# Kernel optimization log

Hardware: AMD Instinct MI355X
Metric: run time of the kernel (lower is better)

Reference implementation:

```python
import jax, jax.numpy as jnp
import numpy as np

EMB = 1024
N_HEAD = 16
HEAD = 64
D_FF = 4 * EMB
LN_EPS = 1e-5


def layernorm(x, g, b):
    mu = jnp.mean(x, axis=-1, keepdims=True)
    var = jnp.mean(jnp.square(x - mu), axis=-1, keepdims=True)
    return (x - mu) * jax.lax.rsqrt(var + LN_EPS) * g + b


def setup_inputs() -> dict:
    key = jax.random.key(0)
    ks = jax.random.split(key, 12)
    s = 0.02
    x = jax.random.normal(ks[0], (4, 2048, EMB), dtype=jnp.float32)
    # per-head Q/K/V projections (no bias), stacked along head axis
    Wq = jax.random.normal(ks[1], (N_HEAD, EMB, HEAD), dtype=jnp.float32) * s
    Wk = jax.random.normal(ks[2], (N_HEAD, EMB, HEAD), dtype=jnp.float32) * s
    Wv = jax.random.normal(ks[3], (N_HEAD, EMB, HEAD), dtype=jnp.float32) * s
    Wo = jax.random.normal(ks[4], (EMB, EMB), dtype=jnp.float32) * s
    bo = jnp.zeros((EMB,), dtype=jnp.float32)
    ln1_g = jnp.ones((EMB,), dtype=jnp.float32)
    ln1_b = jnp.zeros((EMB,), dtype=jnp.float32)
    W1 = jax.random.normal(ks[5], (EMB, D_FF), dtype=jnp.float32) * s
    b1 = jnp.zeros((D_FF,), dtype=jnp.float32)
    W2 = jax.random.normal(ks[6], (D_FF, EMB), dtype=jnp.float32) * s
    b2 = jnp.zeros((EMB,), dtype=jnp.float32)
    ln2_g = jnp.ones((EMB,), dtype=jnp.float32)
    ln2_b = jnp.zeros((EMB,), dtype=jnp.float32)
    return dict(x=x, Wq=Wq, Wk=Wk, Wv=Wv, Wo=Wo, bo=bo, ln1_g=ln1_g,
                ln1_b=ln1_b, W1=W1, b1=b1, W2=W2, b2=b2, ln2_g=ln2_g,
                ln2_b=ln2_b)


def reference(x, Wq, Wk, Wv, Wo, bo, ln1_g, ln1_b, W1, b1, W2, b2, ln2_g, ln2_b):
    B, T, _ = x.shape
    # fused multi-head QKV (equivalent to the per-head Python loop + concat)
    q = jnp.einsum('btd,hdk->bhtk', x, Wq)
    k = jnp.einsum('btd,hdk->bhtk', x, Wk)
    v = jnp.einsum('btd,hdk->bhtk', x, Wv)
    scores = jnp.einsum('bhtk,bhsk->bhts', q, k) / jnp.sqrt(jnp.float32(HEAD))
    att = jax.nn.softmax(scores, axis=-1)
    heads = jnp.einsum('bhts,bhsk->bhtk', att, v)           # [B,H,T,head]
    cat = heads.transpose(0, 2, 1, 3).reshape(B, T, EMB)     # concat over heads
    mha = cat @ Wo + bo
    x = x + layernorm(mha, ln1_g, ln1_b)                     # residual of LN(sublayer)
    ff = jax.nn.gelu(x @ W1 + b1, approximate=False) @ W2 + b2
    x = x + layernorm(ff, ln2_g, ln2_b)
    return x
```

## Files before the change

kernel.cpp:

```cpp
#include <hip/hip_runtime.h>
#include <math.h>


using u16 = unsigned short;
typedef __bf16 bf16x8 __attribute__((ext_vector_type(8)));
typedef __bf16 bf16x4 __attribute__((ext_vector_type(4)));
typedef unsigned short u16x8 __attribute__((ext_vector_type(8)));
typedef unsigned short u16x4 __attribute__((ext_vector_type(4)));
typedef float f32x4 __attribute__((ext_vector_type(4)));

#if defined(__has_builtin)
#if __has_builtin(__builtin_amdgcn_exp2f)
#define EXP2F(x) __builtin_amdgcn_exp2f(x)
#endif
#endif
#ifndef EXP2F
#define EXP2F(x) __expf((x) * 0.69314718055994531f)
#endif

__device__ __forceinline__ float bf2f(u16 h) {
  return __uint_as_float(((unsigned int)h) << 16);
}
__device__ __forceinline__ u16 f2bf(float f) {
  unsigned int u = __float_as_uint(f);
  u += 0x7fffu + ((u >> 16) & 1u);
  return (u16)(u >> 16);
}

__device__ __forceinline__ void gload_lds16(const void* g, void* l) {
  __builtin_amdgcn_global_load_lds(
      (__attribute__((address_space(1))) void*)(g),
      (__attribute__((address_space(3))) void*)(l), 16, 0, 0);
}

__global__ __launch_bounds__(256) void detect_dtype(const u16* __restrict__ x,
                                                    int* __restrict__ flag) {
  __shared__ int cnt[256];
  int c = 0;
#pragma unroll
  for (int j = 0; j < 8; ++j) {
    float v = bf2f(x[threadIdx.x * 8 + j]);
    float a = fabsf(v);
    if (a >= 1e-4f && a <= 64.0f) ++c;
  }
  cnt[threadIdx.x] = c;
  __syncthreads();
  if (threadIdx.x == 0) {
    int t = 0;
    for (int i = 0; i < 256; ++i) t += cnt[i];
    flag[0] = (t < 1638) ? 1 : 0;
  }
}

__global__ __launch_bounds__(256) void cvt_copy(const void* __restrict__ in,
                                                u16* __restrict__ out,
                                                const int* __restrict__ flagp,
                                                long n) {
  long idx = ((long)blockIdx.x * 256 + threadIdx.x) * 4;
  if (idx >= n) return;
  if (*flagp) {
    float4 v = *(const float4*)((const float*)in + idx);
    out[idx] = f2bf(v.x); out[idx + 1] = f2bf(v.y);
    out[idx + 2] = f2bf(v.z); out[idx + 3] = f2bf(v.w);
  } else {
    *(u16x4*)(out + idx) = *(const u16x4*)((const u16*)in + idx);
  }
}

__global__ __launch_bounds__(256) void cvt_vecs(
    const void* s0, const void* s1, const void* s2, const void* s3,
    const void* s4, const void* s5, const void* s6, u16* __restrict__ dst,
    const int* __restrict__ flagp) {
  const int lens[7] = {1024, 1024, 1024, 4096, 1024, 1024, 1024};
  const int offs[7] = {0, 1024, 2048, 3072, 7168, 8192, 9216};
  const void* srcs[7] = {s0, s1, s2, s3, s4, s5, s6};
  int w = blockIdx.x;
  int f = *flagp;
  for (int i = threadIdx.x; i < lens[w]; i += 256)
    dst[offs[w] + i] = f ? f2bf(((const float*)srcs[w])[i])
                         : ((const u16*)srcs[w])[i];
}

__global__ __launch_bounds__(256) void transpose_cvt(
    const void* __restrict__ in, u16* __restrict__ out, int R, int C,
    long inBS, long outBS, const int* __restrict__ flagp) {
  __shared__ u16 tile[32][33];
  int f = *flagp;
  u16* ob = out + (long)blockIdx.z * outBS;
  int c = blockIdx.x * 32 + threadIdx.x;
  int r0 = blockIdx.y * 32;
  if (f) {
    const float* ib = (const float*)in + (long)blockIdx.z * inBS;
#pragma unroll
    for (int i = threadIdx.y; i < 32; i += 8)
      tile[i][threadIdx.x] = f2bf(ib[(long)(r0 + i) * C + c]);
  } else {
    const u16* ib = (const u16*)in + (long)blockIdx.z * inBS;
#pragma unroll
    for (int i = threadIdx.y; i < 32; i += 8)
      tile[i][threadIdx.x] = ib[(long)(r0 + i) * C + c];
  }
  __syncthreads();
  int r = r0 + threadIdx.x;
  int c0 = blockIdx.x * 32;
#pragma unroll
  for (int i = threadIdx.y; i < 32; i += 8)
    ob[(long)(c0 + i) * R + r] = tile[threadIdx.x][i];
}

__global__ __launch_bounds__(256) void kv_frag(const u16* __restrict__ qkv,
                                               u16* __restrict__ KF,
                                               u16* __restrict__ VF) {
  __shared__ u16 Kt[64][72];
  __shared__ u16 Vt[64][72];
  const int jblk = blockIdx.x, bh = blockIdx.y;
  const int b = bh >> 4, h = bh & 15;
  const int tid = threadIdx.x;
  const long j0 = jblk * 64;

  {
    int tt = tid >> 2, c0 = (tid & 3) * 16;
    const u16* src = qkv + (long)(b * 2048 + j0 + tt) * 3072 + h * 64 + c0;
    *(u16x8*)(&Kt[tt][c0]) = *(const u16x8*)(src + 1024);
    *(u16x8*)(&Kt[tt][c0 + 8]) = *(const u16x8*)(src + 1024 + 8);
    *(u16x8*)(&Vt[tt][c0]) = *(const u16x8*)(src + 2048);
    *(u16x8*)(&Vt[tt][c0 + 8]) = *(const u16x8*)(src + 2048 + 8);
  }
  __syncthreads();

  long obase = ((long)bh * 32 + jblk) * 8 * 512;
#pragma unroll
  for (int si = 0; si < 2; ++si) {
    int s = tid * 2 + si;
    int f = s >> 6, ln = s & 63;
    int kt = f >> 2, nt = f & 3;
    int lr = ln & 15, lq = ln >> 4;
    u16x8 ko, vo;
#pragma unroll
    for (int j = 0; j < 8; ++j) {
      ko[j] = Kt[nt * 16 + lr][kt * 32 + lq * 8 + j];
      vo[j] = Vt[kt * 32 + lq * 8 + j][nt * 16 + lr];
    }
    *(u16x8*)(KF + obase + (long)s * 8) = ko;
    *(u16x8*)(VF + obase + (long)s * 8) = vo;
  }
}

template <int EPI>
__global__ __launch_bounds__(256) void gemm_bt(
    const u16* __restrict__ A, const u16* __restrict__ Bt,
    const u16* __restrict__ bias, void* __restrict__ Cout,
    int M, int N, int K) {
  __shared__ u16 As[128 * 32];
  __shared__ u16 Bs[128 * 32];
  const int tid = threadIdx.x;
  const int wave = tid >> 6, lane = tid & 63;
  const int m0 = blockIdx.x * 128, n0 = blockIdx.y * 128;
  const int wm = (wave >> 1) * 64, wn = (wave & 1) * 64;
  const int srow = lane >> 2, skoff = (lane & 3) * 8;

  const u16* ag[2];
  const u16* bg[2];
  u16* al[2];
  u16* bl[2];
#pragma unroll
  for (int p = 0; p < 2; ++p) {
    int r = p * 64 + wave * 16;
    ag[p] = A + (long)(m0 + r + srow) * K + skoff;
    bg[p] = Bt + (long)(n0 + r + srow) * K + skoff;
    al[p] = As + r * 32;
    bl[p] = Bs + r * 32;
  }

  f32x4 acc[4][4] = {};
  const int lr = lane & 15, lk = (lane >> 4) * 8;

  for (int k0 = 0; k0 < K; k0 += 32) {
#pragma unroll
    for (int p = 0; p < 2; ++p) {
      gload_lds16(ag[p] + k0, al[p]);
      gload_lds16(bg[p] + k0, bl[p]);
    }
    __syncthreads();
    bf16x8 af[4], bfr[4];
#pragma unroll
    for (int t = 0; t < 4; ++t) {
      af[t] = *(const bf16x8*)(As + (wm + t * 16 + lr) * 32 + lk);
      bfr[t] = *(const bf16x8*)(Bs + (wn + t * 16 + lr) * 32 + lk);
    }
#pragma unroll
    for (int mt = 0; mt < 4; ++mt)
#pragma unroll
      for (int nt = 0; nt < 4; ++nt)
        acc[mt][nt] = __builtin_amdgcn_mfma_f32_16x16x32_bf16(
            af[mt], bfr[nt], acc[mt][nt], 0, 0, 0);
    __syncthreads();
  }

  const int rq = (lane >> 4) * 4, cl = lane & 15;
#pragma unroll
  for (int mt = 0; mt < 4; ++mt)
#pragma unroll
    for (int nt = 0; nt < 4; ++nt) {
      int col = n0 + wn + nt * 16 + cl;
#pragma unroll
      for (int r = 0; r < 4; ++r) {
        long row = (long)(m0 + wm + mt * 16 + rq + r);
        float v = acc[mt][nt][r];
        if (EPI == 0) {
          ((u16*)Cout)[row * N + col] = f2bf(v);
        } else if (EPI == 2) {
          v += bf2f(bias[col]);
          v = 0.5f * v * (1.0f + erff(v * 0.70710678118654752f));
          ((u16*)Cout)[row * N + col] = f2bf(v);
        } else {
          v += bf2f(bias[col]);
          ((u16*)Cout)[row * N + col] = f2bf(v);
        }
      }
    }
}

__global__ __launch_bounds__(256) void flash_attn(
    const u16* __restrict__ qkv, const u16* __restrict__ KF,
    const u16* __restrict__ VF, u16* __restrict__ cat) {
  const int T = 2048, LD = 3072;
  const float QSCALE = 0.18033688011112042f;
  const float EXPC = 4.3280851226677321f;
  const int bh = blockIdx.y;
  const int b = bh >> 4, h = bh & 15;
  const int tid = threadIdx.x, wave = tid >> 6, lane = tid & 63;
  const int lr = lane & 15, lq = lane >> 4;

  __shared__ u16 Ps[4 * 32 * 72];
  u16* Pw = Ps + wave * 32 * 72;

  const u16* Qb = qkv + (long)(b * 2048) * LD + h * 64;
  const long fbase = (long)bh * 32 * 8 * 512;

  bf16x8 aq[2][2];
#pragma unroll
  for (int st = 0; st < 2; ++st) {
    int qrow = blockIdx.x * 128 + wave * 32 + st * 16 + lr;
#pragma unroll
    for (int kt = 0; kt < 2; ++kt) {
      u16x8 q = *(const u16x8*)(Qb + (long)qrow * LD + kt * 32 + lq * 8);
      bf16x8 t;
#pragma unroll
      for (int j = 0; j < 8; ++j) t[j] = (__bf16)(bf2f(q[j]) * QSCALE);
      aq[st][kt] = t;
    }
  }

  f32x4 o[2][4] = {};
  float lsum[2] = {0.0f, 0.0f};

  for (int jblk = 0; jblk < T / 64; ++jblk) {
    const u16* kf = KF + fbase + (long)jblk * 8 * 512;
    const u16* vf = VF + fbase + (long)jblk * 8 * 512;

    bf16x8 bk[2][4];
#pragma unroll
    for (int kt = 0; kt < 2; ++kt)
#pragma unroll
      for (int nt = 0; nt < 4; ++nt)
        bk[kt][nt] = *(const bf16x8*)(kf + (kt * 4 + nt) * 512 + lane * 8);

    f32x4 s[2][4] = {};
#pragma unroll
    for (int st = 0; st < 2; ++st)
#pragma unroll
      for (int nt = 0; nt < 4; ++nt)
#pragma unroll
        for (int kt = 0; kt < 2; ++kt)
          s[st][nt] = __builtin_amdgcn_mfma_f32_16x16x32_bf16(
              bk[kt][nt], aq[st][kt], s[st][nt], 0, 0, 0);

    bf16x8 bv[2][4];
#pragma unroll
    for (int kt = 0; kt < 2; ++kt)
#pragma unroll
      for (int nt = 0; nt < 4; ++nt)
        bv[kt][nt] = *(const bf16x8*)(vf + (kt * 4 + nt) * 512 + lane * 8);

#pragma unroll
    for (int st = 0; st < 2; ++st)
#pragma unroll
      for (int nt = 0; nt < 4; ++nt) {
        f32x4 p;
#pragma unroll
        for (int r = 0; r < 4; ++r) p[r] = EXP2F(s[st][nt][r] - EXPC);
        lsum[st] += (p[0] + p[1]) + (p[2] + p[3]);
        bf16x4 pk;
#pragma unroll
        for (int r = 0; r < 4; ++r) pk[r] = (__bf16)p[r];
        *(bf16x4*)(Pw + (st * 16 + lr) * 72 + nt * 16 + lq * 4) = pk;
      }

#pragma unroll
    for (int st = 0; st < 2; ++st)
#pragma unroll
      for (int kt = 0; kt < 2; ++kt) {
        bf16x8 ap =
            *(const bf16x8*)(Pw + (st * 16 + lr) * 72 + kt * 32 + lq * 8);
#pragma unroll
        for (int nt = 0; nt < 4; ++nt)
          o[st][nt] = __builtin_amdgcn_mfma_f32_16x16x32_bf16(
              ap, bv[kt][nt], o[st][nt], 0, 0, 0);
      }
  }

#pragma unroll
  for (int st = 0; st < 2; ++st) {
    lsum[st] += __shfl_xor(lsum[st], 16, 64);
    lsum[st] += __shfl_xor(lsum[st], 32, 64);
  }

  u16* ob = cat + (long)(b * 2048) * 1024 + h * 64;
#pragma unroll
  for (int st = 0; st < 2; ++st) {
    int trow = blockIdx.x * 128 + wave * 32 + st * 16 + lq * 4;
#pragma unroll
    for (int r = 0; r < 4; ++r) {
      float linv = 1.0f / __shfl(lsum[st], lq * 4 + r, 64);
#pragma unroll
      for (int nt = 0; nt < 4; ++nt)
        ob[(long)(trow + r) * 1024 + nt * 16 + lr] = f2bf(o[st][nt][r] * linv);
    }
  }
}

__global__ __launch_bounds__(256) void ln_residual(
    const u16* __restrict__ y, const void* __restrict__ res, int res_raw,
    const u16* __restrict__ g, const u16* __restrict__ bb,
    void* __restrict__ out, const int* __restrict__ flagp, int final_out) {
  const long row = blockIdx.x;
  const int tid = threadIdx.x, wave = tid >> 6, lane = tid & 63;
  u16x4 yv = *(const u16x4*)(y + row * 1024 + tid * 4);
  float yy[4];
#pragma unroll
  for (int j = 0; j < 4; ++j) yy[j] = bf2f(yv[j]);
  float s1 = yy[0] + yy[1] + yy[2] + yy[3];
  float s2 = yy[0] * yy[0] + yy[1] * yy[1] + yy[2] * yy[2] + yy[3] * yy[3];
#pragma unroll
  for (int off = 1; off < 64; off <<= 1) {
    s1 += __shfl_xor(s1, off, 64);
    s2 += __shfl_xor(s2, off, 64);
  }
  __shared__ float ws1[4], ws2[4];
  if (lane == 0) { ws1[wave] = s1; ws2[wave] = s2; }
  __syncthreads();
  float t1 = ws1[0] + ws1[1] + ws1[2] + ws1[3];
  float t2 = ws2[0] + ws2[1] + ws2[2] + ws2[3];
  float mu = t1 * (1.0f / 1024.0f);
  float var = t2 * (1.0f / 1024.0f) - mu * mu;
  float rstd = rsqrtf(var + 1e-5f);
  int i = tid * 4;
  bool f32in = res_raw && (*flagp);
  bool f32out = final_out && (*flagp);
#pragma unroll
  for (int j = 0; j < 4; ++j) {
    float rv = f32in ? ((const float*)res)[row * 1024 + i + j]
                     : bf2f(((const u16*)res)[row * 1024 + i + j]);
    float o = rv + (yy[j] - mu) * rstd * bf2f(g[i + j]) + bf2f(bb[i + j]);
    if (f32out)
      ((float*)out)[row * 1024 + i + j] = o;
    else
      ((u16*)out)[row * 1024 + i + j] = f2bf(o);
  }
}

extern "C" void kernel_launch(void* const* d_in, const int* in_sizes, int n_in,
                              void* d_out, int out_size, void* d_ws,
                              size_t ws_size, hipStream_t stream) {
  const void* x_raw = d_in[0];
  const void* Wq = d_in[1];
  const void* Wk = d_in[2];
  const void* Wv = d_in[3];
  const void* Wo = d_in[4];
  const void* bo = d_in[5];
  const void* ln1g = d_in[6];
  const void* ln1b = d_in[7];
  const void* W1 = d_in[8];
  const void* b1 = d_in[9];
  const void* W2 = d_in[10];
  const void* b2 = d_in[11];
  const void* ln2g = d_in[12];
  const void* ln2b = d_in[13];

  char* ws = (char*)d_ws;
  u16* qkv = (u16*)(ws + 0);
  u16* mha = (u16*)(ws + 0);
  u16* h1 = (u16*)(ws + 0);
  u16* cat = (u16*)(ws + 50331648);
  u16* KF = (u16*)(ws + 67108864);
  u16* ff = (u16*)(ws + 67108864);
  u16* xb = (u16*)(ws + 83886080);
  u16* VF = (u16*)(ws + 83886080);
  u16* x1 = (u16*)(ws + 83886080);
  u16* wqkvt = (u16*)(ws + 100663296);
  u16* wot = (u16*)(ws + 106954752);
  u16* w1t = (u16*)(ws + 109051904);
  u16* w2t = (u16*)(ws + 117440512);
  u16* vecs = (u16*)(ws + 125829120);
  int* flag = (int*)(ws + 125853696);

  const u16* v_bo = vecs + 0;
  const u16* v_l1g = vecs + 1024;
  const u16* v_l1b = vecs + 2048;
  const u16* v_b1 = vecs + 3072;
  const u16* v_b2 = vecs + 7168;
  const u16* v_l2g = vecs + 8192;
  const u16* v_l2b = vecs + 9216;

  detect_dtype<<<1, 256, 0, stream>>>((const u16*)x_raw, flag);
  cvt_copy<<<8192, 256, 0, stream>>>(x_raw, xb, flag, 8388608L);
  cvt_vecs<<<7, 256, 0, stream>>>(bo, ln1g, ln1b, b1, b2, ln2g, ln2b, vecs, flag);

  dim3 tb(32, 8);
  transpose_cvt<<<dim3(2, 32, 16), tb, 0, stream>>>(Wq, wqkvt, 1024, 64, 65536, 65536, flag);
  transpose_cvt<<<dim3(2, 32, 16), tb, 0, stream>>>(Wk, wqkvt + 1048576, 1024, 64, 65536, 65536, flag);
  transpose_cvt<<<dim3(2, 32, 16), tb, 0, stream>>>(Wv, wqkvt + 2097152, 1024, 64, 65536, 65536, flag);
  transpose_cvt<<<dim3(32, 32, 1), tb, 0, stream>>>(Wo, wot, 1024, 1024, 0, 0, flag);
  transpose_cvt<<<dim3(128, 32, 1), tb, 0, stream>>>(W1, w1t, 1024, 4096, 0, 0, flag);
  transpose_cvt<<<dim3(32, 128, 1), tb, 0, stream>>>(W2, w2t, 4096, 1024, 0, 0, flag);

  gemm_bt<0><<<dim3(64, 24), 256, 0, stream>>>(xb, wqkvt, nullptr, qkv, 8192, 3072, 1024);
  kv_frag<<<dim3(32, 64), 256, 0, stream>>>(qkv, KF, VF);
  flash_attn<<<dim3(16, 64), 256, 0, stream>>>(qkv, KF, VF, cat);
  gemm_bt<3><<<dim3(64, 8), 256, 0, stream>>>(cat, wot, v_bo, mha, 8192, 1024, 1024);
  ln_residual<<<8192, 256, 0, stream>>>(mha, x_raw, 1, v_l1g, v_l1b, x1, flag, 0);
  gemm_bt<2><<<dim3(64, 32), 256, 0, stream>>>(x1, w1t, v_b1, h1, 8192, 4096, 1024);
  gemm_bt<3><<<dim3(64, 8), 256, 0, stream>>>(h1, w2t, v_b2, ff, 8192, 1024, 4096);
  ln_residual<<<8192, 256, 0, stream>>>(ff, x1, 0, v_l2g, v_l2b, d_out, flag, 1);
}
```

Measured before the change: 656.1 us.

## Replace 128x128 GEMM with double-buffered 256x256 tile GEMM with swizzled LDS

The simple 128x128 single-buffer GEMM is replaced by a 512-thread kernel computing 256x256 output tiles. It uses double-buffered LDS with XOR-swizzled layout, interleaved global-to-LDS staging and MFMA quadrants with explicit barriers and priority hints, and an XCD-aware tile remap. The aim is better operand reuse, fewer LDS bank conflicts and overlap of loads with MFMA work in all four projection GEMMs. The cost is large LDS use (128KB per block), many barriers, and fewer blocks for the N=1024 GEMMs (128 tiles), which may underfill the GPU's CUs.

```diff
diff --git a/kernel.cpp b/kernel.cpp
--- a/kernel.cpp
+++ b/kernel.cpp
@@ -146,77 +146,158 @@
   }
 }
 
+__device__ __forceinline__ bf16x8 fragld(const u16* lb, int row, int ks,
+                                         int lq) {
+  int slot = ((ks << 2) | lq) ^ (row & 7);
+  return *(const bf16x8*)(lb + row * 64 + slot * 8);
+}
+
+#define BARX __builtin_amdgcn_s_barrier()
+#define LGKM0                                          \
+  do {                                                 \
+    asm volatile("s_waitcnt lgkmcnt(0)" ::: "memory"); \
+    __builtin_amdgcn_sched_barrier(0);                 \
+  } while (0)
+
+#define RDA(BASE, HH)                                                     \
+  _Pragma("unroll") for (int mf = 0; mf < 4; ++mf) {                      \
+    _Pragma("unroll") for (int ks = 0; ks < 2; ++ks)                      \
+        a_[mf][ks] = fragld(BASE, wm + (HH)*64 + mf * 16 + lr, ks, lq);   \
+  }
+#define RDB(BASE, GG, DST)                                                \
+  _Pragma("unroll") for (int nf = 0; nf < 2; ++nf) {                      \
+    _Pragma("unroll") for (int ks = 0; ks < 2; ++ks)                      \
+        DST[nf][ks] = fragld(BASE, wn + (GG)*32 + nf * 16 + lr, ks, lq);  \
+  }
+#define MFMA_Q(HH, GG, BSRC)                                              \
+  __builtin_amdgcn_s_setprio(1);                                          \
+  _Pragma("unroll") for (int mf = 0; mf < 4; ++mf) {                      \
+    _Pragma("unroll") for (int nf = 0; nf < 2; ++nf) {                    \
+      _Pragma("unroll") for (int ks = 0; ks < 2; ++ks)                    \
+          acc[(HH)*4 + mf][(GG)*2 + nf] =                                 \
+              __builtin_amdgcn_mfma_f32_16x16x32_bf16(                    \
+                  a_[mf][ks], BSRC[nf][ks],                               \
+                  acc[(HH)*4 + mf][(GG)*2 + nf], 0, 0, 0);                \
+    }                                                                     \
+  }                                                                       \
+  __builtin_amdgcn_s_setprio(0)
+
 template <int EPI>
-__global__ __launch_bounds__(256) void gemm_bt(
+__global__ __launch_bounds__(512, 2) void gemm256(
     const u16* __restrict__ A, const u16* __restrict__ Bt,
-    const u16* __restrict__ bias, void* __restrict__ Cout,
+    const u16* __restrict__ bias, u16* __restrict__ Cout,
     int M, int N, int K) {
-  __shared__ u16 As[128 * 32];
-  __shared__ u16 Bs[128 * 32];
+  __shared__ u16 lds[2][2][16384];
   const int tid = threadIdx.x;
   const int wave = tid >> 6, lane = tid & 63;
-  const int m0 = blockIdx.x * 128, n0 = blockIdx.y * 128;
-  const int wm = (wave >> 1) * 64, wn = (wave & 1) * 64;
-  const int srow = lane >> 2, skoff = (lane & 3) * 8;
-
-  const u16* ag[2];
-  const u16* bg[2];
-  u16* al[2];
-  u16* bl[2];
-#pragma unroll
-  for (int p = 0; p < 2; ++p) {
-    int r = p * 64 + wave * 16;
-    ag[p] = A + (long)(m0 + r + srow) * K + skoff;
-    bg[p] = Bt + (long)(n0 + r + srow) * K + skoff;
-    al[p] = As + r * 32;
-    bl[p] = Bs + r * 32;
-  }
-
-  f32x4 acc[4][4] = {};
-  const int lr = lane & 15, lk = (lane >> 4) * 8;
-
-  for (int k0 = 0; k0 < K; k0 += 32) {
-#pragma unroll
-    for (int p = 0; p < 2; ++p) {
-      gload_lds16(ag[p] + k0, al[p]);
-      gload_lds16(bg[p] + k0, bl[p]);
-    }
-    __syncthreads();
-    bf16x8 af[4], bfr[4];
-#pragma unroll
-    for (int t = 0; t < 4; ++t) {
-      af[t] = *(const bf16x8*)(As + (wm + t * 16 + lr) * 32 + lk);
-      bfr[t] = *(const bf16x8*)(Bs + (wn + t * 16 + lr) * 32 + lk);
-    }
-#pragma unroll
-    for (int mt = 0; mt < 4; ++mt)
-#pragma unroll
-      for (int nt = 0; nt < 4; ++nt)
-        acc[mt][nt] = __builtin_amdgcn_mfma_f32_16x16x32_bf16(
-            af[mt], bfr[nt], acc[mt][nt], 0, 0, 0);
-    __syncthreads();
-  }
-
-  const int rq = (lane >> 4) * 4, cl = lane & 15;
-#pragma unroll
-  for (int mt = 0; mt < 4; ++mt)
-#pragma unroll
-    for (int nt = 0; nt < 4; ++nt) {
-      int col = n0 + wn + nt * 16 + cl;
+  const int lr = lane & 15, lq = lane >> 4;
+
+  const int MT = M >> 8, NT = N >> 8;
+  const int nwg = MT * NT;
+  int wg = blockIdx.x;
+  if (!(nwg & 7)) wg = (wg & 7) * (nwg >> 3) + (wg >> 3);
+  const int tm = wg % MT, tn = wg / MT;
+  const long m0 = (long)tm << 8, n0 = (long)tn << 8;
+
+  const int wm = (wave >> 2) << 7;
+  const int wn = (wave & 3) << 6;
+
+  const int srow = lane >> 3;
+  const int sslot = (lane & 7) ^ srow;
+  const long arow = (m0 + wave * 8 + srow) * (long)K + sslot * 8;
+  const long brow = (n0 + wave * 8 + srow) * (long)K + sslot * 8;
+
+  u16* const A0p = &lds[0][0][0];
+  u16* const B0p = &lds[0][1][0];
+  u16* const A1p = &lds[1][0][0];
+  u16* const B1p = &lds[1][1][0];
+
+  auto stage = [&](const u16* g, u16* l, int tau, int hh, long rowoff) {
+    const u16* src = g + rowoff + (long)hh * 128 * K + (long)tau * 64;
+    u16* dst = l + hh * 8192 + (wave << 9);
+    gload_lds16(src, dst);
+    gload_lds16(src + ((long)K << 6), dst + 4096);
+  };
+
+  stage(Bt, B0p, 0, 0, brow);
+  stage(Bt, B0p, 0, 1, brow);
+  stage(A, A0p, 0, 0, arow);
+  stage(A, A0p, 0, 1, arow);
+  stage(Bt, B1p, 1, 0, brow);
+  stage(Bt, B1p, 1, 1, brow);
+  asm volatile("s_waitcnt vmcnt(4)" ::: "memory");
+  BARX;
+
+  f32x4 acc[8][4] = {};
+  const int KT = K >> 6, NP = KT >> 1;
+
+  for (int i = 0; i < NP; ++i) {
+    const int ta = 2 * i, tb = ta + 1;
+    const bool nl = (i + 1 < NP);
+    bf16x8 a_[4][2], b0_[2][2], b1_[2][2];
+
+    RDA(A0p, 0);
+    RDB(B0p, 0, b0_);
+    stage(A, A1p, tb, 0, arow);
+    BARX; LGKM0;
+    MFMA_Q(0, 0, b0_);
+    BARX;
+    RDB(B0p, 1, b1_);
+    stage(A, A1p, tb, 1, arow);
+    BARX; LGKM0;
+    MFMA_Q(0, 1, b1_);
+    BARX;
+    RDA(A0p, 1);
+    if (nl) stage(Bt, B0p, ta + 2, 0, brow);
+    BARX; LGKM0;
+    MFMA_Q(1, 1, b1_);
+    BARX;
+    if (nl) stage(Bt, B0p, ta + 2, 1, brow);
+    BARX; LGKM0;
+    MFMA_Q(1, 0, b0_);
+    if (nl) asm volatile("s_waitcnt vmcnt(4)" ::: "memory");
+    else    asm volatile("s_waitcnt vmcnt(0)" ::: "memory");
+    BARX;
+    RDA(A1p, 0);
+    RDB(B1p, 0, b0_);
+    if (nl) stage(A, A0p, ta + 2, 0, arow);
+    BARX; LGKM0;
+    MFMA_Q(0, 0, b0_);
+    BARX;
+    RDB(B1p, 1, b1_);
+    if (nl) stage(A, A0p, ta + 2, 1, arow);
+    BARX; LGKM0;
+    MFMA_Q(0, 1, b1_);
+    BARX;
+    RDA(A1p, 1);
+    if (nl) stage(Bt, B1p, tb + 2, 0, brow);
+    BARX; LGKM0;
+    MFMA_Q(1, 1, b1_);
+    BARX;
+    if (nl) stage(Bt, B1p, tb + 2, 1, brow);
+    BARX; LGKM0;
+    MFMA_Q(1, 0, b0_);
+    if (nl) asm volatile("s_waitcnt vmcnt(4)" ::: "memory");
+    BARX;
+  }
+
+  const int rq = lq * 4;
+#pragma unroll
+  for (int mf = 0; mf < 8; ++mf)
+#pragma unroll
+    for (int nf = 0; nf < 4; ++nf) {
+      const int col = (int)n0 + wn + nf * 16 + lr;
 #pragma unroll
       for (int r = 0; r < 4; ++r) {
-        long row = (long)(m0 + wm + mt * 16 + rq + r);
-        float v = acc[mt][nt][r];
-        if (EPI == 0) {
-          ((u16*)Cout)[row * N + col] = f2bf(v);
-        } else if (EPI == 2) {
+        const long row = m0 + wm + mf * 16 + rq + r;
+        float v = acc[mf][nf][r];
+        if (EPI == 2) {
           v += bf2f(bias[col]);
           v = 0.5f * v * (1.0f + erff(v * 0.70710678118654752f));
-          ((u16*)Cout)[row * N + col] = f2bf(v);
-        } else {
+        } else if (EPI == 3) {
           v += bf2f(bias[col]);
-          ((u16*)Cout)[row * N + col] = f2bf(v);
         }
+        Cout[row * (long)N + col] = f2bf(v);
       }
     }
 }
@@ -425,12 +506,12 @@
   transpose_cvt<<<dim3(128, 32, 1), tb, 0, stream>>>(W1, w1t, 1024, 4096, 0, 0, flag);
   transpose_cvt<<<dim3(32, 128, 1), tb, 0, stream>>>(W2, w2t, 4096, 1024, 0, 0, flag);
 
-  gemm_bt<0><<<dim3(64, 24), 256, 0, stream>>>(xb, wqkvt, nullptr, qkv, 8192, 3072, 1024);
+  gemm256<0><<<384, 512, 0, stream>>>(xb, wqkvt, nullptr, qkv, 8192, 3072, 1024);
   kv_frag<<<dim3(32, 64), 256, 0, stream>>>(qkv, KF, VF);
   flash_attn<<<dim3(16, 64), 256, 0, stream>>>(qkv, KF, VF, cat);
-  gemm_bt<3><<<dim3(64, 8), 256, 0, stream>>>(cat, wot, v_bo, mha, 8192, 1024, 1024);
+  gemm256<3><<<128, 512, 0, stream>>>(cat, wot, v_bo, mha, 8192, 1024, 1024);
   ln_residual<<<8192, 256, 0, stream>>>(mha, x_raw, 1, v_l1g, v_l1b, x1, flag, 0);
-  gemm_bt<2><<<dim3(64, 32), 256, 0, stream>>>(x1, w1t, v_b1, h1, 8192, 4096, 1024);
-  gemm_bt<3><<<dim3(64, 8), 256, 0, stream>>>(h1, w2t, v_b2, ff, 8192, 1024, 4096);
+  gemm256<2><<<512, 512, 0, stream>>>(x1, w1t, v_b1, h1, 8192, 4096, 1024);
+  gemm256<3><<<128, 512, 0, stream>>>(h1, w2t, v_b2, ff, 8192, 1024, 4096);
   ln_residual<<<8192, 256, 0, stream>>>(ff, x1, 0, v_l2g, v_l2b, d_out, flag, 1);
 }
```

After: 726.1 us. 10.7% more time.

## Replace GEMM with double-buffered 256-row tiled kernel using swizzled LDS

Applied to the files above, without the earlier changes.

Replaces the 128x128, K=32, single-buffered GEMM with a 512-thread kernel that computes 256xBN tiles over K=64 steps. LDS is double-buffered so the next tile's global-to-LDS loads are issued before the current tile's MFMAs. Fragment reads use an XOR swizzle to avoid LDS bank conflicts, and workgroup IDs are remapped to group tiles for better L2 reuse. The larger tiles raise register and LDS pressure and leave fewer workgroups for the N=1024 GEMMs (256 blocks).

```diff
diff --git a/kernel.cpp b/kernel.cpp
--- a/kernel.cpp
+++ b/kernel.cpp
@@ -146,77 +146,139 @@
   }
 }
 
-template <int EPI>
-__global__ __launch_bounds__(256) void gemm_bt(
+__device__ __forceinline__ bf16x8 fragld(const u16* lb, int row, int ks,
+                                         int lq) {
+  int slot = ((ks << 2) | lq) ^ (row & 7);
+  return *(const bf16x8*)(lb + row * 64 + slot * 8);
+}
+
+template <int EPI, int BN>
+__global__ __launch_bounds__(512, 2) void gemm2ph(
     const u16* __restrict__ A, const u16* __restrict__ Bt,
-    const u16* __restrict__ bias, void* __restrict__ Cout,
+    const u16* __restrict__ bias, u16* __restrict__ Cout,
     int M, int N, int K) {
-  __shared__ u16 As[128 * 32];
-  __shared__ u16 Bs[128 * 32];
+  static_assert(BN == 256 || BN == 128, "");
+  constexpr int NFQ = BN / 128;
+  __shared__ u16 As[2][16384];
+  __shared__ u16 Bs[2][BN * 64];
   const int tid = threadIdx.x;
   const int wave = tid >> 6, lane = tid & 63;
-  const int m0 = blockIdx.x * 128, n0 = blockIdx.y * 128;
-  const int wm = (wave >> 1) * 64, wn = (wave & 1) * 64;
-  const int srow = lane >> 2, skoff = (lane & 3) * 8;
-
-  const u16* ag[2];
-  const u16* bg[2];
-  u16* al[2];
-  u16* bl[2];
-#pragma unroll
-  for (int p = 0; p < 2; ++p) {
-    int r = p * 64 + wave * 16;
-    ag[p] = A + (long)(m0 + r + srow) * K + skoff;
-    bg[p] = Bt + (long)(n0 + r + srow) * K + skoff;
-    al[p] = As + r * 32;
-    bl[p] = Bs + r * 32;
-  }
-
-  f32x4 acc[4][4] = {};
-  const int lr = lane & 15, lk = (lane >> 4) * 8;
-
-  for (int k0 = 0; k0 < K; k0 += 32) {
-#pragma unroll
-    for (int p = 0; p < 2; ++p) {
-      gload_lds16(ag[p] + k0, al[p]);
-      gload_lds16(bg[p] + k0, bl[p]);
-    }
+  const int lr = lane & 15, lq = lane >> 4;
+
+  const int MT = M >> 8, NTt = N / BN;
+  const int nwg = MT * NTt;
+  int wg = blockIdx.x;
+  if (!(nwg & 7)) wg = (wg & 7) * (nwg >> 3) + (wg >> 3);
+  const int tm = wg % MT, tn = wg / MT;
+  const long m0 = (long)tm << 8;
+  const long n0 = (long)tn * BN;
+
+  const int wm = (wave >> 2) << 7;
+  const int wn = (wave & 3) * (BN / 4);
+
+  const int srow = lane >> 3;
+  const int skoff = ((lane & 7) ^ srow) * 8;
+
+  auto stage = [&](int buf, int t) {
+#pragma unroll
+    for (int j = 0; j < 4; ++j)
+      gload_lds16(
+          A + (m0 + j * 64 + wave * 8 + srow) * (long)K + t * 64 + skoff,
+          &As[buf][j * 4096 + (wave << 9)]);
+#pragma unroll
+    for (int j = 0; j < BN / 64; ++j)
+      gload_lds16(
+          Bt + (n0 + j * 64 + wave * 8 + srow) * (long)K + t * 64 + skoff,
+          &Bs[buf][j * 4096 + (wave << 9)]);
+  };
+
+  f32x4 acc[8][2 * NFQ] = {};
+  const int NT = K >> 6;
+  int cur = 0;
+
+  stage(0, 0);
+  __syncthreads();
+
+  for (int t = 0; t < NT; ++t) {
+    const u16* Ab = As[cur];
+    const u16* Bb = Bs[cur];
+    if (t + 1 < NT) stage(cur ^ 1, t + 1);
+
+    bf16x8 a_[4][2], b0_[NFQ][2], b1_[NFQ][2];
+#pragma unroll
+    for (int mf = 0; mf < 4; ++mf)
+#pragma unroll
+      for (int ks = 0; ks < 2; ++ks)
+        a_[mf][ks] = fragld(Ab, wm + mf * 16 + lr, ks, lq);
+#pragma unroll
+    for (int nf = 0; nf < NFQ; ++nf)
+#pragma unroll
+      for (int ks = 0; ks < 2; ++ks)
+        b0_[nf][ks] = fragld(Bb, wn + nf * 16 + lr, ks, lq);
+#pragma unroll
+    for (int mf = 0; mf < 4; ++mf)
+#pragma unroll
+      for (int nf = 0; nf < NFQ; ++nf)
+#pragma unroll
+        for (int ks = 0; ks < 2; ++ks)
+          acc[mf][nf] = __builtin_amdgcn_mfma_f32_16x16x32_bf16(
+              a_[mf][ks], b0_[nf][ks], acc[mf][nf], 0, 0, 0);
+#pragma unroll
+    for (int nf = 0; nf < NFQ; ++nf)
+#pragma unroll
+      for (int ks = 0; ks < 2; ++ks)
+        b1_[nf][ks] = fragld(Bb, wn + BN / 8 + nf * 16 + lr, ks, lq);
+#pragma unroll
+    for (int mf = 0; mf < 4; ++mf)
+#pragma unroll
+      for (int nf = 0; nf < NFQ; ++nf)
+#pragma unroll
+        for (int ks = 0; ks < 2; ++ks)
+          acc[mf][NFQ + nf] = __builtin_amdgcn_mfma_f32_16x16x32_bf16(
+              a_[mf][ks], b1_[nf][ks], acc[mf][NFQ + nf], 0, 0, 0);
+#pragma unroll
+    for (int mf = 0; mf < 4; ++mf)
+#pragma unroll
+      for (int ks = 0; ks < 2; ++ks)
+        a_[mf][ks] = fragld(Ab, wm + 64 + mf * 16 + lr, ks, lq);
+#pragma unroll
+    for (int mf = 0; mf < 4; ++mf)
+#pragma unroll
+      for (int nf = 0; nf < NFQ; ++nf)
+#pragma unroll
+        for (int ks = 0; ks < 2; ++ks)
+          acc[4 + mf][NFQ + nf] = __builtin_amdgcn_mfma_f32_16x16x32_bf16(
+              a_[mf][ks], b1_[nf][ks], acc[4 + mf][NFQ + nf], 0, 0, 0);
+#pragma unroll
+    for (int mf = 0; mf < 4; ++mf)
+#pragma unroll
+      for (int nf = 0; nf < NFQ; ++nf)
+#pragma unroll
+        for (int ks = 0; ks < 2; ++ks)
+          acc[4 + mf][nf] = __builtin_amdgcn_mfma_f32_16x16x32_bf16(
+              a_[mf][ks], b0_[nf][ks], acc[4 + mf][nf], 0, 0, 0);
+
     __syncthreads();
-    bf16x8 af[4], bfr[4];
-#pragma unroll
-    for (int t = 0; t < 4; ++t) {
-      af[t] = *(const bf16x8*)(As + (wm + t * 16 + lr) * 32 + lk);
-      bfr[t] = *(const bf16x8*)(Bs + (wn + t * 16 + lr) * 32 + lk);
-    }
-#pragma unroll
-    for (int mt = 0; mt < 4; ++mt)
-#pragma unroll
-      for (int nt = 0; nt < 4; ++nt)
-        acc[mt][nt] = __builtin_amdgcn_mfma_f32_16x16x32_bf16(
-            af[mt], bfr[nt], acc[mt][nt], 0, 0, 0);
-    __syncthreads();
-  }
-
-  const int rq = (lane >> 4) * 4, cl = lane & 15;
-#pragma unroll
-  for (int mt = 0; mt < 4; ++mt)
-#pragma unroll
-    for (int nt = 0; nt < 4; ++nt) {
-      int col = n0 + wn + nt * 16 + cl;
+    cur ^= 1;
+  }
+
+  const int rq = lq * 4;
+#pragma unroll
+  for (int mf = 0; mf < 8; ++mf)
+#pragma unroll
+    for (int nf2 = 0; nf2 < 2 * NFQ; ++nf2) {
+      const int col = (int)n0 + wn + nf2 * 16 + lr;
 #pragma unroll
       for (int r = 0; r < 4; ++r) {
-        long row = (long)(m0 + wm + mt * 16 + rq + r);
-        float v = acc[mt][nt][r];
-        if (EPI == 0) {
-          ((u16*)Cout)[row * N + col] = f2bf(v);
-        } else if (EPI == 2) {
+        const long row = m0 + wm + mf * 16 + rq + r;
+        float v = acc[mf][nf2][r];
+        if (EPI == 2) {
           v += bf2f(bias[col]);
           v = 0.5f * v * (1.0f + erff(v * 0.70710678118654752f));
-          ((u16*)Cout)[row * N + col] = f2bf(v);
-        } else {
+        } else if (EPI == 3) {
           v += bf2f(bias[col]);
-          ((u16*)Cout)[row * N + col] = f2bf(v);
         }
+        Cout[row * (long)N + col] = f2bf(v);
       }
     }
 }
@@ -425,12 +487,12 @@
   transpose_cvt<<<dim3(128, 32, 1), tb, 0, stream>>>(W1, w1t, 1024, 4096, 0, 0, flag);
   transpose_cvt<<<dim3(32, 128, 1), tb, 0, stream>>>(W2, w2t, 4096, 1024, 0, 0, flag);
 
-  gemm_bt<0><<<dim3(64, 24), 256, 0, stream>>>(xb, wqkvt, nullptr, qkv, 8192, 3072, 1024);
+  gemm2ph<0, 256><<<384, 512, 0, stream>>>(xb, wqkvt, nullptr, qkv, 8192, 3072, 1024);
   kv_frag<<<dim3(32, 64), 256, 0, stream>>>(qkv, KF, VF);
   flash_attn<<<dim3(16, 64), 256, 0, stream>>>(qkv, KF, VF, cat);
-  gemm_bt<3><<<dim3(64, 8), 256, 0, stream>>>(cat, wot, v_bo, mha, 8192, 1024, 1024);
+  gemm2ph<3, 128><<<256, 512, 0, stream>>>(cat, wot, v_bo, mha, 8192, 1024, 1024);
   ln_residual<<<8192, 256, 0, stream>>>(mha, x_raw, 1, v_l1g, v_l1b, x1, flag, 0);
-  gemm_bt<2><<<dim3(64, 32), 256, 0, stream>>>(x1, w1t, v_b1, h1, 8192, 4096, 1024);
-  gemm_bt<3><<<dim3(64, 8), 256, 0, stream>>>(h1, w2t, v_b2, ff, 8192, 1024, 4096);
+  gemm2ph<2, 256><<<512, 512, 0, stream>>>(x1, w1t, v_b1, h1, 8192, 4096, 1024);
+  gemm2ph<3, 128><<<256, 512, 0, stream>>>(h1, w2t, v_b2, ff, 8192, 1024, 4096);
   ln_residual<<<8192, 256, 0, stream>>>(ff, x1, 0, v_l2g, v_l2b, d_out, flag, 1);
 }
```

New measurement: 633.8 us. -3.4%, faster.
